# Performance work log

Measured on AMD Instinct MI355X. Metric: run time of the kernel, lower is better.

The kernel has to match this reference:

```python
import jax, jax.numpy as jnp
import numpy as np

HEAD_DIM = 128
HIDDEN = 5120
NUM_KV_GROUPS = 8
NUM_MODALITIES = 3
NUM_Q_HEADS = 40
QKV_PER_MOD = NUM_Q_HEADS * HEAD_DIM + 2 * NUM_KV_GROUPS * HEAD_DIM + NUM_Q_HEADS  # 7208


def _rms_norm(x, w, eps=1e-6):
    xf = x.astype(jnp.float32)
    inv = jax.lax.rsqrt(jnp.mean(xf * xf, axis=-1, keepdims=True) + eps)
    return (xf * inv).astype(x.dtype) * w


def _apply_rope(x, cos, sin):
    # x: [B,S,H,D], cos/sin: [B,S,rd]
    rd = cos.shape[-1]
    xr, xp = x[..., :rd], x[..., rd:]
    c, s = cos[:, :, None, :], sin[:, :, None, :]
    x1, x2 = xr[..., : rd // 2], xr[..., rd // 2:]
    rot = jnp.concatenate([-x2, x1], axis=-1)
    return jnp.concatenate([xr * c + rot * s, xp], axis=-1)


def setup_inputs() -> dict:
    key = jax.random.key(0)
    ks = jax.random.split(key, 6)
    B, S = 1, 2048
    return {
        "x": jax.random.normal(ks[0], (B, S, HIDDEN), jnp.float32),
        "rope_cos": jax.random.uniform(ks[1], (B, S, HEAD_DIM), jnp.float32),
        "rope_sin": jax.random.uniform(ks[2], (B, S, HEAD_DIM), jnp.float32),
        "modality_ids": jax.random.randint(ks[3], (B, S), 0, NUM_MODALITIES, jnp.int32),
        "pre_norm": jnp.ones((NUM_MODALITIES * HIDDEN,), jnp.float32),
        "qkv_w": jax.random.normal(ks[4], (NUM_MODALITIES * QKV_PER_MOD, HIDDEN), jnp.float32) * 0.02,
        "q_norm": jnp.ones((NUM_MODALITIES * HEAD_DIM,), jnp.float32),
        "k_norm": jnp.ones((NUM_MODALITIES * HEAD_DIM,), jnp.float32),
        "proj_w": jax.random.normal(ks[5], (NUM_MODALITIES * HIDDEN, HIDDEN), jnp.float32) * 0.02,
    }


def reference(x, rope_cos, rope_sin, modality_ids, pre_norm, qkv_w, q_norm, k_norm, proj_w):
    B, S, _ = x.shape
    # per-token modality gather of pre-norm weight
    norm_w = pre_norm.reshape(NUM_MODALITIES, HIDDEN)[modality_ids]  # [B,S,H]
    normed = _rms_norm(x, norm_w)

    # modality-routed QKV: compute all modalities, select with one-hot (dense, jit-friendly)
    oh = jax.nn.one_hot(modality_ids, NUM_MODALITIES, dtype=x.dtype)  # [B,S,M]
    qkv_w3 = qkv_w.reshape(NUM_MODALITIES, QKV_PER_MOD, HIDDEN)
    qkv_all = jnp.einsum("bsh,moh->bsmo", normed, qkv_w3)  # [B,S,M,QKV]
    qkv = jnp.einsum("bsm,bsmo->bso", oh, qkv_all)

    q_dim = NUM_Q_HEADS * HEAD_DIM
    k_dim = NUM_KV_GROUPS * HEAD_DIM
    q = qkv[..., :q_dim].reshape(B, S, NUM_Q_HEADS, HEAD_DIM)
    k = qkv[..., q_dim:q_dim + k_dim].reshape(B, S, NUM_KV_GROUPS, HEAD_DIM)
    v = qkv[..., q_dim + k_dim:q_dim + 2 * k_dim].reshape(B, S, NUM_KV_GROUPS, HEAD_DIM)
    gate = jax.nn.sigmoid(qkv[..., q_dim + 2 * k_dim:q_dim + 2 * k_dim + NUM_Q_HEADS])  # [B,S,NQ]

    qn = q_norm.reshape(NUM_MODALITIES, HEAD_DIM)[modality_ids][:, :, None, :]  # [B,S,1,D]
    kn = k_norm.reshape(NUM_MODALITIES, HEAD_DIM)[modality_ids][:, :, None, :]
    q = _rms_norm(q, qn)
    k = _rms_norm(k, kn)

    q = _apply_rope(q, rope_cos, rope_sin)
    k = _apply_rope(k, rope_cos, rope_sin)

    repeat = NUM_Q_HEADS // NUM_KV_GROUPS
    k = jnp.repeat(k, repeat, axis=2)  # [B,S,NQ,D]
    v = jnp.repeat(v, repeat, axis=2)

    scale = 1.0 / np.sqrt(HEAD_DIM)
    scores = jnp.einsum("bqhd,bkhd->bhqk", q, k) * scale  # [B,NQ,S,S]
    attn = jax.nn.softmax(scores, axis=-1)
    out = jnp.einsum("bhqk,bkhd->bqhd", attn, v)  # [B,S,NQ,D]

    out = (out * gate[..., None]).reshape(B, S, NUM_Q_HEADS * HEAD_DIM)

    proj_w3 = proj_w.reshape(NUM_MODALITIES, HIDDEN, HIDDEN)
    proj_all = jnp.einsum("bsh,moh->bsmo", out, proj_w3)  # [B,S,M,H]
    return jnp.einsum("bsm,bsmo->bso", oh, proj_all)
```

## Files before the change

kernel.cpp:

```cpp
#include <hip/hip_runtime.h>

typedef _Float16 f16;
typedef f16 f16x8 __attribute__((ext_vector_type(8)));
typedef f16 f16x4 __attribute__((ext_vector_type(4)));
typedef float f32x4 __attribute__((ext_vector_type(4)));

#define HID 5120
#define QKVO 7208
#define S_TOK 2048
#define NQH 40
#define NKV 8
#define HD 128

__device__ __forceinline__ void gload16(const void* g, void* l) {
    __builtin_amdgcn_global_load_lds(
        (const __attribute__((address_space(1))) void*)g,
        (__attribute__((address_space(3))) void*)l,
        16, 0, 0);
}

__global__ void sort_tokens(const int* __restrict__ mod, int* __restrict__ sorted,
                            int* __restrict__ offs)
{
    int tid = threadIdx.x, wave = tid >> 6, lane = tid & 63;
    int mloc[8];
    int c[3] = {0, 0, 0};
#pragma unroll
    for (int j = 0; j < 8; ++j) {
        int m = mod[tid * 8 + j];
        mloc[j] = m;
        c[m]++;
    }
    __shared__ int wsum[4][3];
    int excl[3];
#pragma unroll
    for (int m = 0; m < 3; ++m) {
        int v = c[m];
        int incl = v;
        for (int d = 1; d < 64; d <<= 1) {
            int n = __shfl_up(incl, d, 64);
            if (lane >= d) incl += n;
        }
        excl[m] = incl - v;
        if (lane == 63) wsum[wave][m] = incl;
    }
    __syncthreads();
    int wbase[3], tot[3];
#pragma unroll
    for (int m = 0; m < 3; ++m) {
        int b = 0, t = 0;
        for (int w = 0; w < 4; ++w) {
            if (w < wave) b += wsum[w][m];
            t += wsum[w][m];
        }
        wbase[m] = b;
        tot[m] = t;
    }
    int base[3];
    base[0] = 0;
    base[1] = tot[0];
    base[2] = tot[0] + tot[1];
    if (tid == 0) {
        offs[0] = 0;
        offs[1] = tot[0];
        offs[2] = tot[0] + tot[1];
        offs[3] = S_TOK;
    }
    int pos[3];
#pragma unroll
    for (int m = 0; m < 3; ++m) pos[m] = base[m] + wbase[m] + excl[m];
#pragma unroll
    for (int j = 0; j < 8; ++j) {
        int m = mloc[j];
        sorted[pos[m]++] = tid * 8 + j;
    }
}

__global__ void cvt_f32_f16(const float* __restrict__ src, f16* __restrict__ dst, int n4)
{
    int i = blockIdx.x * 256 + threadIdx.x;
    int stride = gridDim.x * 256;
    const float4* s4 = (const float4*)src;
    f16x4* d4 = (f16x4*)dst;
    for (; i < n4; i += stride) {
        float4 a = s4[i];
        f16x4 h;
        h[0] = (f16)a.x; h[1] = (f16)a.y; h[2] = (f16)a.z; h[3] = (f16)a.w;
        d4[i] = h;
    }
}

__global__ void rms_pre(const float* __restrict__ x, const int* __restrict__ mod,
                        const float* __restrict__ prenorm, f16* __restrict__ A1)
{
    int tok = blockIdx.x, tid = threadIdx.x;
    int m = mod[tok];
    const float4* xv = (const float4*)(x + (size_t)tok * HID);
    float4 v[5];
    float ss = 0.f;
#pragma unroll
    for (int j = 0; j < 5; ++j) {
        v[j] = xv[tid + 256 * j];
        ss += v[j].x * v[j].x + v[j].y * v[j].y + v[j].z * v[j].z + v[j].w * v[j].w;
    }
    for (int d = 1; d < 64; d <<= 1) ss += __shfl_xor(ss, d, 64);
    __shared__ float ws[4];
    if ((tid & 63) == 0) ws[tid >> 6] = ss;
    __syncthreads();
    float tot = ws[0] + ws[1] + ws[2] + ws[3];
    float inv = rsqrtf(tot * (1.f / HID) + 1e-6f);
    const float4* wv = (const float4*)(prenorm + (size_t)m * HID);
    f16x4* out4 = (f16x4*)(A1 + (size_t)tok * HID);
#pragma unroll
    for (int j = 0; j < 5; ++j) {
        float4 w = wv[tid + 256 * j];
        f16x4 h;
        h[0] = (f16)(v[j].x * inv * w.x);
        h[1] = (f16)(v[j].y * inv * w.y);
        h[2] = (f16)(v[j].z * inv * w.z);
        h[3] = (f16)(v[j].w * inv * w.w);
        out4[tid + 256 * j] = h;
    }
}

__global__ void gemm_grouped(const f16* __restrict__ A, const f16* __restrict__ W,
                             float* __restrict__ C,
                             const int* __restrict__ sorted_tok,
                             const int* __restrict__ mod_off, int NW, int NTN, int NPAN)
{
    const int K = HID;
    int F = blockIdx.x;
    int g = F & 7, s = F >> 3;
    int P = (s >> 4) * 8 + g;
    if (P >= NPAN) return;
    int mt = s & 15;
    int nt = P % NTN, mod = P / NTN;
    int off = mod_off[mod], cnt = mod_off[mod + 1] - off;
    if (mt * 128 >= cnt) return;
    __shared__ __align__(16) f16 As[128 * 64];
    __shared__ __align__(16) f16 Bs[128 * 64];
    __shared__ int rowtok[128];
    int tid = threadIdx.x, wave = tid >> 6, lane = tid & 63;
    if (tid < 128) {
        int r = mt * 128 + tid;
        rowtok[tid] = (r < cnt) ? sorted_tok[off + r] : -1;
    }
    __syncthreads();
    int wr = wave >> 1, wc = wave & 1;
    f32x4 acc[4][4] = {};
    const f16* Wm = W + (size_t)mod * NW * K;
    for (int kt = 0; kt < K / 64; ++kt) {
        int k0 = kt * 64;
#pragma unroll
        for (int it = 0; it < 4; ++it) {
            int c = it * 256 + tid;
            int row = c >> 3, kc = c & 7, skc = kc ^ (row & 7);
            int tk = rowtok[row];
            if (tk < 0) tk = 0;
            gload16(A + (size_t)tk * K + k0 + skc * 8, &As[c * 8]);
        }
#pragma unroll
        for (int it = 0; it < 4; ++it) {
            int c = it * 256 + tid;
            int row = c >> 3, kc = c & 7, skc = kc ^ (row & 7);
            int o = nt * 128 + row;
            if (o >= NW) o = NW - 1;
            gload16(Wm + (size_t)o * K + k0 + skc * 8, &Bs[c * 8]);
        }
        __syncthreads();
#pragma unroll
        for (int ks = 0; ks < 2; ++ks) {
            f16x8 a[4], b[4];
#pragma unroll
            for (int i = 0; i < 4; ++i) {
                int ar = wr * 64 + i * 16 + (lane & 15);
                int ac = (ks * 4 + (lane >> 4)) ^ (ar & 7);
                a[i] = *(const f16x8*)&As[ar * 64 + ac * 8];
                int br = wc * 64 + i * 16 + (lane & 15);
                int bc = (ks * 4 + (lane >> 4)) ^ (br & 7);
                b[i] = *(const f16x8*)&Bs[br * 64 + bc * 8];
            }
#pragma unroll
            for (int mi = 0; mi < 4; ++mi)
#pragma unroll
                for (int nj = 0; nj < 4; ++nj)
                    acc[mi][nj] = __builtin_amdgcn_mfma_f32_16x16x32_f16(
                        a[mi], b[nj], acc[mi][nj], 0, 0, 0);
        }
        __syncthreads();
    }
    int cl = lane & 15, rg = lane >> 4;
#pragma unroll
    for (int mi = 0; mi < 4; ++mi) {
#pragma unroll
        for (int rr = 0; rr < 4; ++rr) {
            int row = wr * 64 + mi * 16 + rg * 4 + rr;
            int tk = rowtok[row];
            if (tk < 0) continue;
            float* crow = C + (size_t)tk * NW;
#pragma unroll
            for (int nj = 0; nj < 4; ++nj) {
                int o = nt * 128 + wc * 64 + nj * 16 + cl;
                if (o < NW) crow[o] = acc[mi][nj][rr];
            }
        }
    }
}

__global__ void qkv_post(const float* __restrict__ qkv, const int* __restrict__ mod,
                         const float* __restrict__ cosb, const float* __restrict__ sinb,
                         const float* __restrict__ qnorm, const float* __restrict__ knorm,
                         f16* __restrict__ Qb, f16* __restrict__ Kb, float* __restrict__ gateb)
{
    int tok = blockIdx.x, tid = threadIdx.x;
    int wave = tid >> 6, lane = tid & 63;
    int m = mod[tok];
    float c0 = cosb[tok * HD + lane], c1 = cosb[tok * HD + 64 + lane];
    float s0 = sinb[tok * HD + lane], s1 = sinb[tok * HD + 64 + lane];
    const float* row = qkv + (size_t)tok * QKVO;
    for (int u = wave; u < 48; u += 4) {
        int base = (u < 40) ? u * HD : NQH * HD + (u - 40) * HD;
        float x0 = row[base + lane];
        float x1 = row[base + 64 + lane];
        float ss = x0 * x0 + x1 * x1;
        for (int d = 1; d < 64; d <<= 1) ss += __shfl_xor(ss, d, 64);
        float inv = rsqrtf(ss * (1.f / HD) + 1e-6f);
        const float* nw = (u < 40 ? qnorm : knorm) + m * HD;
        float n0 = x0 * inv * nw[lane];
        float n1 = x1 * inv * nw[64 + lane];
        float r0 = n0 * c0 - n1 * s0;
        float r1 = n1 * c1 + n0 * s1;
        if (u < 40) {
            const float sc = 0.08838834764831845f;
            r0 *= sc; r1 *= sc;
            Qb[((size_t)u * S_TOK + tok) * HD + lane] = (f16)r0;
            Qb[((size_t)u * S_TOK + tok) * HD + 64 + lane] = (f16)r1;
        } else {
            Kb[((size_t)(u - 40) * S_TOK + tok) * HD + lane] = (f16)r0;
            Kb[((size_t)(u - 40) * S_TOK + tok) * HD + 64 + lane] = (f16)r1;
        }
    }
    if (tid < 40) {
        float g = row[NQH * HD + 2 * NKV * HD + tid];
        gateb[tok * 40 + tid] = 1.f / (1.f + __expf(-g));
    }
}

__global__ void vtrans(const float* __restrict__ qkv, f16* __restrict__ Vt)
{
    int tc = blockIdx.x;
    int g = blockIdx.y;
    int tid = threadIdx.x;
    __shared__ float tile[64][129];
#pragma unroll
    for (int it = 0; it < 8; ++it) {
        int idx = it * 256 + tid;
        int r = idx >> 5, c4 = idx & 31;
        float4 v = *(const float4*)(qkv + (size_t)(tc * 64 + r) * QKVO + NQH * HD + NKV * HD + g * HD + c4 * 4);
        tile[r][c4 * 4 + 0] = v.x;
        tile[r][c4 * 4 + 1] = v.y;
        tile[r][c4 * 4 + 2] = v.z;
        tile[r][c4 * 4 + 3] = v.w;
    }
    __syncthreads();
    int d = tid >> 1, half = tid & 1;
    f16* dst = Vt + ((size_t)g * HD + d) * S_TOK + tc * 64 + half * 32;
#pragma unroll
    for (int j = 0; j < 32; ++j) dst[j] = (f16)tile[half * 32 + j][d];
}

__global__ void attn(const f16* __restrict__ Qb, const f16* __restrict__ Kb,
                     const f16* __restrict__ Vtb, const float* __restrict__ gateb,
                     f16* __restrict__ A2)
{
    int qt = blockIdx.x, h = blockIdx.y, grp = h / 5;
    int tid = threadIdx.x, wave = tid >> 6, lane = tid & 63;
    __shared__ __align__(16) char smem[73728];
    f16* Qs  = (f16*)smem;
    f16* Kb0 = (f16*)(smem + 16384);
    f16* Kb1 = (f16*)smem;
    f16* Vb0 = (f16*)(smem + 32768);
    f16* Vb1 = (f16*)(smem + 49152);
    char* pbase = smem + 65536 + wave * 2048;

    const f16* Qg = Qb + ((size_t)h * S_TOK + qt * 64) * HD;
    const f16* Kg = Kb + (size_t)grp * S_TOK * HD;
    const f16* Vg = Vtb + (size_t)grp * HD * S_TOK;

#pragma unroll
    for (int it = 0; it < 4; ++it) {
        int c = it * 256 + tid, row = c >> 4, kc = c & 15, skc = kc ^ (row & 15);
        gload16(Qg + row * HD + skc * 8, &Qs[c * 8]);
    }
#pragma unroll
    for (int it = 0; it < 4; ++it) {
        int c = it * 256 + tid, row = c >> 4, kc = c & 15, skc = kc ^ (row & 15);
        gload16(Kg + (size_t)row * HD + skc * 8, &Kb0[c * 8]);
    }
#pragma unroll
    for (int it = 0; it < 4; ++it) {
        int c = it * 256 + tid, row = c >> 3, kc = c & 7, skc = kc ^ (row & 7);
        gload16(Vg + (size_t)row * S_TOK + skc * 8, &Vb0[c * 8]);
    }
    asm volatile("s_waitcnt vmcnt(8)" ::: "memory");
    __builtin_amdgcn_s_barrier();
    f16x8 qf[4];
    {
        int row = wave * 16 + (lane & 15);
#pragma unroll
        for (int ks = 0; ks < 4; ++ks) {
            int sk = (ks * 4 + (lane >> 4)) ^ (row & 15);
            qf[ks] = *(const f16x8*)&Qs[row * 128 + sk * 8];
        }
    }
    asm volatile("s_waitcnt lgkmcnt(0)" ::: "memory");
    __builtin_amdgcn_s_barrier();

    f32x4 o[8] = {};
    float mrow[4] = {-3.0e38f, -3.0e38f, -3.0e38f, -3.0e38f};
    float lrow[4] = {0.f, 0.f, 0.f, 0.f};

    int cur = 0;
    for (int t = 0; t < 32; ++t) {
        f16* Ks = cur ? Kb1 : Kb0;
        f16* Vs = cur ? Vb1 : Vb0;
        if (t < 31) {
            f16* Kn = cur ? Kb0 : Kb1;
            f16* Vn = cur ? Vb0 : Vb1;
#pragma unroll
            for (int it = 0; it < 4; ++it) {
                int c = it * 256 + tid, row = c >> 4, kc = c & 15, skc = kc ^ (row & 15);
                gload16(Kg + (size_t)((t + 1) * 64 + row) * HD + skc * 8, &Kn[c * 8]);
            }
#pragma unroll
            for (int it = 0; it < 4; ++it) {
                int c = it * 256 + tid, row = c >> 3, kc = c & 7, skc = kc ^ (row & 7);
                gload16(Vg + (size_t)row * S_TOK + (t + 1) * 64 + skc * 8, &Vn[c * 8]);
            }
            asm volatile("s_waitcnt vmcnt(8)" ::: "memory");
        } else {
            asm volatile("s_waitcnt vmcnt(0)" ::: "memory");
        }
        __builtin_amdgcn_s_barrier();

        f32x4 s[4] = {};
#pragma unroll
        for (int ks = 0; ks < 4; ++ks) {
#pragma unroll
            for (int nj = 0; nj < 4; ++nj) {
                int kr = nj * 16 + (lane & 15);
                int sk = (ks * 4 + (lane >> 4)) ^ (kr & 15);
                f16x8 kf = *(const f16x8*)&Ks[kr * 128 + sk * 8];
                s[nj] = __builtin_amdgcn_mfma_f32_16x16x32_f16(qf[ks], kf, s[nj], 0, 0, 0);
            }
        }
        float mx[4], corr[4], psum[4];
#pragma unroll
        for (int r = 0; r < 4; ++r)
            mx[r] = fmaxf(fmaxf(s[0][r], s[1][r]), fmaxf(s[2][r], s[3][r]));
        for (int d = 1; d < 16; d <<= 1) {
#pragma unroll
            for (int r = 0; r < 4; ++r) mx[r] = fmaxf(mx[r], __shfl_xor(mx[r], d, 16));
        }
#pragma unroll
        for (int r = 0; r < 4; ++r) {
            float mn = fmaxf(mrow[r], mx[r]);
            corr[r] = __expf(mrow[r] - mn);
            mrow[r] = mn;
            psum[r] = 0.f;
        }
#pragma unroll
        for (int nj = 0; nj < 4; ++nj) {
#pragma unroll
            for (int r = 0; r < 4; ++r) {
                float p = __expf(s[nj][r] - mrow[r]);
                psum[r] += p;
                int prow = (lane >> 4) * 4 + r, col = (lane & 15) + nj * 16;
                int addr = (prow * 128 + col * 2) ^ ((prow & 7) << 4);
                *(f16*)(pbase + addr) = (f16)p;
            }
        }
        for (int d = 1; d < 16; d <<= 1) {
#pragma unroll
            for (int r = 0; r < 4; ++r) psum[r] += __shfl_xor(psum[r], d, 16);
        }
#pragma unroll
        for (int r = 0; r < 4; ++r) lrow[r] = lrow[r] * corr[r] + psum[r];
#pragma unroll
        for (int nj2 = 0; nj2 < 8; ++nj2)
#pragma unroll
            for (int r = 0; r < 4; ++r) o[nj2][r] *= corr[r];
#pragma unroll
        for (int ks2 = 0; ks2 < 2; ++ks2) {
            int prow = lane & 15;
            int sk = (ks2 * 4 + (lane >> 4)) ^ (prow & 7);
            f16x8 pa = *(const f16x8*)(pbase + prow * 128 + sk * 16);
#pragma unroll
            for (int nj2 = 0; nj2 < 8; ++nj2) {
                int vr = nj2 * 16 + (lane & 15);
                int skv = (ks2 * 4 + (lane >> 4)) ^ (vr & 7);
                f16x8 vf = *(const f16x8*)&Vs[vr * 64 + skv * 8];
                o[nj2] = __builtin_amdgcn_mfma_f32_16x16x32_f16(pa, vf, o[nj2], 0, 0, 0);
            }
        }
        asm volatile("s_waitcnt lgkmcnt(0)" ::: "memory");
        __builtin_amdgcn_s_barrier();
        cur ^= 1;
    }
    int rbase = qt * 64 + wave * 16 + (lane >> 4) * 4;
#pragma unroll
    for (int r = 0; r < 4; ++r) {
        int tok = rbase + r;
        float sc = gateb[tok * 40 + h] / lrow[r];
#pragma unroll
        for (int nj2 = 0; nj2 < 8; ++nj2) {
            int d = nj2 * 16 + (lane & 15);
            A2[(size_t)tok * HID + h * HD + d] = (f16)(o[nj2][r] * sc);
        }
    }
}

extern "C" void kernel_launch(void* const* d_in, const int* in_sizes, int n_in,
                              void* d_out, int out_size, void* d_ws, size_t ws_size,
                              hipStream_t stream)
{
    const float* x = (const float*)d_in[0];
    const float* rc = (const float*)d_in[1];
    const float* rs = (const float*)d_in[2];
    const int* mod = (const int*)d_in[3];
    const float* prenorm = (const float*)d_in[4];
    const float* qkvw = (const float*)d_in[5];
    const float* qn = (const float*)d_in[6];
    const float* kn = (const float*)d_in[7];
    const float* projw = (const float*)d_in[8];
    float* out = (float*)d_out;

    char* p = (char*)d_ws;
    auto alloc = [&](size_t bytes) {
        char* r = p;
        p += (bytes + 255) & ~(size_t)255;
        return r;
    };
    int* sorted = (int*)alloc(S_TOK * 4);
    int* offs = (int*)alloc(16);
    f16* A1 = (f16*)alloc((size_t)S_TOK * HID * 2);
    f16* Wq = (f16*)alloc((size_t)3 * QKVO * HID * 2);
    f16* Wp = (f16*)alloc((size_t)3 * HID * HID * 2);
    float* qkv = (float*)alloc((size_t)S_TOK * QKVO * 4);
    f16* Qb = (f16*)alloc((size_t)NQH * S_TOK * HD * 2);
    f16* Kb = (f16*)alloc((size_t)NKV * S_TOK * HD * 2);
    f16* Vt = (f16*)alloc((size_t)NKV * HD * S_TOK * 2);
    float* gate = (float*)alloc((size_t)S_TOK * 40 * 4);
    f16* A2 = (f16*)alloc((size_t)S_TOK * HID * 2);
    if ((size_t)(p - (char*)d_ws) > ws_size) return;

    sort_tokens<<<1, 256, 0, stream>>>(mod, sorted, offs);
    cvt_f32_f16<<<2048, 256, 0, stream>>>(qkvw, Wq, 3 * QKVO * HID / 4);
    cvt_f32_f16<<<2048, 256, 0, stream>>>(projw, Wp, 3 * HID * HID / 4);
    rms_pre<<<2048, 256, 0, stream>>>(x, mod, prenorm, A1);
    {
        int NTN = 57, NPAN = NTN * 3;
        int grid = 8 * ((NPAN + 7) / 8) * 16;
        gemm_grouped<<<grid, 256, 0, stream>>>(A1, Wq, qkv, sorted, offs, QKVO, NTN, NPAN);
    }
    qkv_post<<<2048, 256, 0, stream>>>(qkv, mod, rc, rs, qn, kn, Qb, Kb, gate);
    vtrans<<<dim3(32, 8), 256, 0, stream>>>(qkv, Vt);
    attn<<<dim3(32, 40), 256, 0, stream>>>(Qb, Kb, Vt, gate, A2);
    {
        int NTN = 40, NPAN = NTN * 3;
        int grid = 8 * ((NPAN + 7) / 8) * 16;
        gemm_grouped<<<grid, 256, 0, stream>>>(A2, Wp, out, sorted, offs, HID, NTN, NPAN);
    }
}
```

Before: 914.0 us.

## Enlarge grouped GEMM tiles to 256x256, lazily rescale softmax, vectorize P stores

The grouped GEMM moves from 128x128 tiles with 256 threads to 256x256 tiles with 512 threads, and each wave now holds an 8x4 MFMA accumulator block. This raises arithmetic intensity per loaded tile and cuts redundant global loads. The attention kernel skips the running-max rescale unless the new max exceeds the old one by more than 8, and writes P as f16x4 vectors with a permuted column layout. The vtrans output order is changed to match that layout. The risks are register pressure from the 128-float accumulators, lower occupancy, more wasted work on partial tiles, and fp16 overflow headroom in P from the lazy rescale.

```diff
diff --git a/kernel.cpp b/kernel.cpp
--- a/kernel.cpp
+++ b/kernel.cpp
@@ -123,37 +123,38 @@
     }
 }
 
-__global__ void gemm_grouped(const f16* __restrict__ A, const f16* __restrict__ W,
-                             float* __restrict__ C,
-                             const int* __restrict__ sorted_tok,
-                             const int* __restrict__ mod_off, int NW, int NTN, int NPAN)
+__global__ __launch_bounds__(512, 2) void gemm_grouped(
+    const f16* __restrict__ A, const f16* __restrict__ W,
+    float* __restrict__ C,
+    const int* __restrict__ sorted_tok,
+    const int* __restrict__ mod_off, int NW, int NTN, int NPAN)
 {
     const int K = HID;
     int F = blockIdx.x;
     int g = F & 7, s = F >> 3;
-    int P = (s >> 4) * 8 + g;
+    int P = (s >> 3) * 8 + g;
     if (P >= NPAN) return;
-    int mt = s & 15;
+    int mt = s & 7;
     int nt = P % NTN, mod = P / NTN;
     int off = mod_off[mod], cnt = mod_off[mod + 1] - off;
-    if (mt * 128 >= cnt) return;
-    __shared__ __align__(16) f16 As[128 * 64];
-    __shared__ __align__(16) f16 Bs[128 * 64];
-    __shared__ int rowtok[128];
+    if (mt * 256 >= cnt) return;
+    __shared__ __align__(16) f16 As[256 * 64];
+    __shared__ __align__(16) f16 Bs[256 * 64];
+    __shared__ int rowtok[256];
     int tid = threadIdx.x, wave = tid >> 6, lane = tid & 63;
-    if (tid < 128) {
-        int r = mt * 128 + tid;
+    if (tid < 256) {
+        int r = mt * 256 + tid;
         rowtok[tid] = (r < cnt) ? sorted_tok[off + r] : -1;
     }
     __syncthreads();
-    int wr = wave >> 1, wc = wave & 1;
-    f32x4 acc[4][4] = {};
+    int wr = wave >> 2, wc = wave & 3;
+    f32x4 acc[8][4] = {};
     const f16* Wm = W + (size_t)mod * NW * K;
     for (int kt = 0; kt < K / 64; ++kt) {
         int k0 = kt * 64;
 #pragma unroll
         for (int it = 0; it < 4; ++it) {
-            int c = it * 256 + tid;
+            int c = it * 512 + tid;
             int row = c >> 3, kc = c & 7, skc = kc ^ (row & 7);
             int tk = rowtok[row];
             if (tk < 0) tk = 0;
@@ -161,27 +162,30 @@
         }
 #pragma unroll
         for (int it = 0; it < 4; ++it) {
-            int c = it * 256 + tid;
+            int c = it * 512 + tid;
             int row = c >> 3, kc = c & 7, skc = kc ^ (row & 7);
-            int o = nt * 128 + row;
+            int o = nt * 256 + row;
             if (o >= NW) o = NW - 1;
             gload16(Wm + (size_t)o * K + k0 + skc * 8, &Bs[c * 8]);
         }
         __syncthreads();
 #pragma unroll
         for (int ks = 0; ks < 2; ++ks) {
-            f16x8 a[4], b[4];
-#pragma unroll
-            for (int i = 0; i < 4; ++i) {
-                int ar = wr * 64 + i * 16 + (lane & 15);
+            f16x8 a[8], b[4];
+#pragma unroll
+            for (int i = 0; i < 8; ++i) {
+                int ar = wr * 128 + i * 16 + (lane & 15);
                 int ac = (ks * 4 + (lane >> 4)) ^ (ar & 7);
                 a[i] = *(const f16x8*)&As[ar * 64 + ac * 8];
-                int br = wc * 64 + i * 16 + (lane & 15);
+            }
+#pragma unroll
+            for (int j = 0; j < 4; ++j) {
+                int br = wc * 64 + j * 16 + (lane & 15);
                 int bc = (ks * 4 + (lane >> 4)) ^ (br & 7);
-                b[i] = *(const f16x8*)&Bs[br * 64 + bc * 8];
-            }
-#pragma unroll
-            for (int mi = 0; mi < 4; ++mi)
+                b[j] = *(const f16x8*)&Bs[br * 64 + bc * 8];
+            }
+#pragma unroll
+            for (int mi = 0; mi < 8; ++mi)
 #pragma unroll
                 for (int nj = 0; nj < 4; ++nj)
                     acc[mi][nj] = __builtin_amdgcn_mfma_f32_16x16x32_f16(
@@ -191,16 +195,16 @@
     }
     int cl = lane & 15, rg = lane >> 4;
 #pragma unroll
-    for (int mi = 0; mi < 4; ++mi) {
+    for (int mi = 0; mi < 8; ++mi) {
 #pragma unroll
         for (int rr = 0; rr < 4; ++rr) {
-            int row = wr * 64 + mi * 16 + rg * 4 + rr;
+            int row = wr * 128 + mi * 16 + rg * 4 + rr;
             int tk = rowtok[row];
             if (tk < 0) continue;
             float* crow = C + (size_t)tk * NW;
 #pragma unroll
             for (int nj = 0; nj < 4; ++nj) {
-                int o = nt * 128 + wc * 64 + nj * 16 + cl;
+                int o = nt * 256 + wc * 64 + nj * 16 + cl;
                 if (o < NW) crow[o] = acc[mi][nj][rr];
             }
         }
@@ -264,9 +268,12 @@
     }
     __syncthreads();
     int d = tid >> 1, half = tid & 1;
-    f16* dst = Vt + ((size_t)g * HD + d) * S_TOK + tc * 64 + half * 32;
-#pragma unroll
-    for (int j = 0; j < 32; ++j) dst[j] = (f16)tile[half * 32 + j][d];
+    f16* dst = Vt + ((size_t)g * HD + d) * S_TOK + tc * 64;
+#pragma unroll
+    for (int j = 0; j < 32; ++j) {
+        int c = half * 32 + j;
+        dst[c] = (f16)tile[16 * (c & 3) + (c >> 2)][d];
+    }
 }
 
 __global__ void attn(const f16* __restrict__ Qb, const f16* __restrict__ Kb,
@@ -354,7 +361,7 @@
                 s[nj] = __builtin_amdgcn_mfma_f32_16x16x32_f16(qf[ks], kf, s[nj], 0, 0, 0);
             }
         }
-        float mx[4], corr[4], psum[4];
+        float mx[4], psum[4];
 #pragma unroll
         for (int r = 0; r < 4; ++r)
             mx[r] = fmaxf(fmaxf(s[0][r], s[1][r]), fmaxf(s[2][r], s[3][r]));
@@ -362,34 +369,41 @@
 #pragma unroll
             for (int r = 0; r < 4; ++r) mx[r] = fmaxf(mx[r], __shfl_xor(mx[r], d, 16));
         }
+        bool need = false;
+#pragma unroll
+        for (int r = 0; r < 4; ++r) need = need || (mx[r] > mrow[r] + 8.f);
+        if (__any(need)) {
+#pragma unroll
+            for (int r = 0; r < 4; ++r) {
+                float nm = fmaxf(mrow[r], mx[r]);
+                float corr = __expf(mrow[r] - nm);
+                mrow[r] = nm;
+                lrow[r] *= corr;
+#pragma unroll
+                for (int nj2 = 0; nj2 < 8; ++nj2) o[nj2][r] *= corr;
+            }
+        }
+#pragma unroll
+        for (int r = 0; r < 4; ++r) psum[r] = 0.f;
 #pragma unroll
         for (int r = 0; r < 4; ++r) {
-            float mn = fmaxf(mrow[r], mx[r]);
-            corr[r] = __expf(mrow[r] - mn);
-            mrow[r] = mn;
-            psum[r] = 0.f;
-        }
-#pragma unroll
-        for (int nj = 0; nj < 4; ++nj) {
-#pragma unroll
-            for (int r = 0; r < 4; ++r) {
+            f16x4 hp;
+#pragma unroll
+            for (int nj = 0; nj < 4; ++nj) {
                 float p = __expf(s[nj][r] - mrow[r]);
                 psum[r] += p;
-                int prow = (lane >> 4) * 4 + r, col = (lane & 15) + nj * 16;
-                int addr = (prow * 128 + col * 2) ^ ((prow & 7) << 4);
-                *(f16*)(pbase + addr) = (f16)p;
-            }
+                hp[nj] = (f16)p;
+            }
+            int q = (lane >> 4) * 4 + r;
+            int addr = q * 128 + ((8 * (lane & 15)) ^ ((q & 7) << 4));
+            *(f16x4*)(pbase + addr) = hp;
         }
         for (int d = 1; d < 16; d <<= 1) {
 #pragma unroll
             for (int r = 0; r < 4; ++r) psum[r] += __shfl_xor(psum[r], d, 16);
         }
 #pragma unroll
-        for (int r = 0; r < 4; ++r) lrow[r] = lrow[r] * corr[r] + psum[r];
-#pragma unroll
-        for (int nj2 = 0; nj2 < 8; ++nj2)
-#pragma unroll
-            for (int r = 0; r < 4; ++r) o[nj2][r] *= corr[r];
+        for (int r = 0; r < 4; ++r) lrow[r] += psum[r];
 #pragma unroll
         for (int ks2 = 0; ks2 < 2; ++ks2) {
             int prow = lane & 15;
@@ -459,16 +473,16 @@
     cvt_f32_f16<<<2048, 256, 0, stream>>>(projw, Wp, 3 * HID * HID / 4);
     rms_pre<<<2048, 256, 0, stream>>>(x, mod, prenorm, A1);
     {
-        int NTN = 57, NPAN = NTN * 3;
-        int grid = 8 * ((NPAN + 7) / 8) * 16;
-        gemm_grouped<<<grid, 256, 0, stream>>>(A1, Wq, qkv, sorted, offs, QKVO, NTN, NPAN);
+        int NTN = (QKVO + 255) / 256, NPAN = NTN * 3;
+        int grid = ((NPAN + 7) / 8) * 8 * 8;
+        gemm_grouped<<<grid, 512, 0, stream>>>(A1, Wq, qkv, sorted, offs, QKVO, NTN, NPAN);
     }
     qkv_post<<<2048, 256, 0, stream>>>(qkv, mod, rc, rs, qn, kn, Qb, Kb, gate);
     vtrans<<<dim3(32, 8), 256, 0, stream>>>(qkv, Vt);
     attn<<<dim3(32, 40), 256, 0, stream>>>(Qb, Kb, Vt, gate, A2);
     {
-        int NTN = 40, NPAN = NTN * 3;
-        int grid = 8 * ((NPAN + 7) / 8) * 16;
-        gemm_grouped<<<grid, 256, 0, stream>>>(A2, Wp, out, sorted, offs, HID, NTN, NPAN);
-    }
-}
+        int NTN = HID / 256, NPAN = NTN * 3;
+        int grid = ((NPAN + 7) / 8) * 8 * 8;
+        gemm_grouped<<<grid, 512, 0, stream>>>(A2, Wp, out, sorted, offs, HID, NTN, NPAN);
+    }
+}
```

Result: slower. 1.079 ms (+18.1%).

## Load fp32 weights directly in GEMM, lazy softmax rescale, vectorize P stores

Applied to the files above, without the earlier changes.

Drops the separate fp32-to-fp16 weight conversion kernels; the grouped GEMM now streams fp32 weights into shared memory and converts to fp16 when loading fragments, removing a full read/write pass over both weight tensors. Attention only rescales the running max and accumulators when the row max grows by more than a threshold, and writes P as packed f16x4 with a changed column layout. vtrans writes V columns in a permuted token order to match the new P layout. The costs are doubled shared memory and global traffic per B tile in the GEMM, repeated weight conversion by every M-tile that reuses a panel, and a layout coupling between vtrans and the attention P writes.

```diff
diff --git a/kernel.cpp b/kernel.cpp
--- a/kernel.cpp
+++ b/kernel.cpp
@@ -76,20 +76,6 @@
     }
 }
 
-__global__ void cvt_f32_f16(const float* __restrict__ src, f16* __restrict__ dst, int n4)
-{
-    int i = blockIdx.x * 256 + threadIdx.x;
-    int stride = gridDim.x * 256;
-    const float4* s4 = (const float4*)src;
-    f16x4* d4 = (f16x4*)dst;
-    for (; i < n4; i += stride) {
-        float4 a = s4[i];
-        f16x4 h;
-        h[0] = (f16)a.x; h[1] = (f16)a.y; h[2] = (f16)a.z; h[3] = (f16)a.w;
-        d4[i] = h;
-    }
-}
-
 __global__ void rms_pre(const float* __restrict__ x, const int* __restrict__ mod,
                         const float* __restrict__ prenorm, f16* __restrict__ A1)
 {
@@ -123,7 +109,7 @@
     }
 }
 
-__global__ void gemm_grouped(const f16* __restrict__ A, const f16* __restrict__ W,
+__global__ void gemm_grouped(const f16* __restrict__ A, const float* __restrict__ W,
                              float* __restrict__ C,
                              const int* __restrict__ sorted_tok,
                              const int* __restrict__ mod_off, int NW, int NTN, int NPAN)
@@ -138,7 +124,7 @@
     int off = mod_off[mod], cnt = mod_off[mod + 1] - off;
     if (mt * 128 >= cnt) return;
     __shared__ __align__(16) f16 As[128 * 64];
-    __shared__ __align__(16) f16 Bs[128 * 64];
+    __shared__ __align__(16) float Bsf[128 * 64];
     __shared__ int rowtok[128];
     int tid = threadIdx.x, wave = tid >> 6, lane = tid & 63;
     if (tid < 128) {
@@ -148,7 +134,7 @@
     __syncthreads();
     int wr = wave >> 1, wc = wave & 1;
     f32x4 acc[4][4] = {};
-    const f16* Wm = W + (size_t)mod * NW * K;
+    const float* Wm = W + (size_t)mod * NW * K;
     for (int kt = 0; kt < K / 64; ++kt) {
         int k0 = kt * 64;
 #pragma unroll
@@ -160,12 +146,12 @@
             gload16(A + (size_t)tk * K + k0 + skc * 8, &As[c * 8]);
         }
 #pragma unroll
-        for (int it = 0; it < 4; ++it) {
+        for (int it = 0; it < 8; ++it) {
             int c = it * 256 + tid;
-            int row = c >> 3, kc = c & 7, skc = kc ^ (row & 7);
+            int row = c >> 4, kc = c & 15, skc = kc ^ (row & 15);
             int o = nt * 128 + row;
             if (o >= NW) o = NW - 1;
-            gload16(Wm + (size_t)o * K + k0 + skc * 8, &Bs[c * 8]);
+            gload16(Wm + (size_t)o * K + k0 + skc * 4, &Bsf[c * 4]);
         }
         __syncthreads();
 #pragma unroll
@@ -176,9 +162,19 @@
                 int ar = wr * 64 + i * 16 + (lane & 15);
                 int ac = (ks * 4 + (lane >> 4)) ^ (ar & 7);
                 a[i] = *(const f16x8*)&As[ar * 64 + ac * 8];
-                int br = wc * 64 + i * 16 + (lane & 15);
-                int bc = (ks * 4 + (lane >> 4)) ^ (br & 7);
-                b[i] = *(const f16x8*)&Bs[br * 64 + bc * 8];
+            }
+#pragma unroll
+            for (int j = 0; j < 4; ++j) {
+                int br = wc * 64 + j * 16 + (lane & 15);
+                int ch = ks * 4 + (lane >> 4);
+                int s0 = (2 * ch) ^ (br & 15);
+                int s1 = (2 * ch + 1) ^ (br & 15);
+                float4 lo = *(const float4*)&Bsf[br * 64 + s0 * 4];
+                float4 hi = *(const float4*)&Bsf[br * 64 + s1 * 4];
+                f16x8 h;
+                h[0] = (f16)lo.x; h[1] = (f16)lo.y; h[2] = (f16)lo.z; h[3] = (f16)lo.w;
+                h[4] = (f16)hi.x; h[5] = (f16)hi.y; h[6] = (f16)hi.z; h[7] = (f16)hi.w;
+                b[j] = h;
             }
 #pragma unroll
             for (int mi = 0; mi < 4; ++mi)
@@ -264,9 +260,12 @@
     }
     __syncthreads();
     int d = tid >> 1, half = tid & 1;
-    f16* dst = Vt + ((size_t)g * HD + d) * S_TOK + tc * 64 + half * 32;
-#pragma unroll
-    for (int j = 0; j < 32; ++j) dst[j] = (f16)tile[half * 32 + j][d];
+    f16* dst = Vt + ((size_t)g * HD + d) * S_TOK + tc * 64;
+#pragma unroll
+    for (int j = 0; j < 32; ++j) {
+        int c = half * 32 + j;
+        dst[c] = (f16)tile[16 * (c & 3) + (c >> 2)][d];
+    }
 }
 
 __global__ void attn(const f16* __restrict__ Qb, const f16* __restrict__ Kb,
@@ -354,7 +353,7 @@
                 s[nj] = __builtin_amdgcn_mfma_f32_16x16x32_f16(qf[ks], kf, s[nj], 0, 0, 0);
             }
         }
-        float mx[4], corr[4], psum[4];
+        float mx[4], psum[4];
 #pragma unroll
         for (int r = 0; r < 4; ++r)
             mx[r] = fmaxf(fmaxf(s[0][r], s[1][r]), fmaxf(s[2][r], s[3][r]));
@@ -362,34 +361,41 @@
 #pragma unroll
             for (int r = 0; r < 4; ++r) mx[r] = fmaxf(mx[r], __shfl_xor(mx[r], d, 16));
         }
+        bool need = false;
+#pragma unroll
+        for (int r = 0; r < 4; ++r) need = need || (mx[r] > mrow[r] + 8.f);
+        if (__any(need)) {
+#pragma unroll
+            for (int r = 0; r < 4; ++r) {
+                float nm = fmaxf(mrow[r], mx[r]);
+                float corr = __expf(mrow[r] - nm);
+                mrow[r] = nm;
+                lrow[r] *= corr;
+#pragma unroll
+                for (int nj2 = 0; nj2 < 8; ++nj2) o[nj2][r] *= corr;
+            }
+        }
+#pragma unroll
+        for (int r = 0; r < 4; ++r) psum[r] = 0.f;
 #pragma unroll
         for (int r = 0; r < 4; ++r) {
-            float mn = fmaxf(mrow[r], mx[r]);
-            corr[r] = __expf(mrow[r] - mn);
-            mrow[r] = mn;
-            psum[r] = 0.f;
-        }
-#pragma unroll
-        for (int nj = 0; nj < 4; ++nj) {
-#pragma unroll
-            for (int r = 0; r < 4; ++r) {
+            f16x4 hp;
+#pragma unroll
+            for (int nj = 0; nj < 4; ++nj) {
                 float p = __expf(s[nj][r] - mrow[r]);
                 psum[r] += p;
-                int prow = (lane >> 4) * 4 + r, col = (lane & 15) + nj * 16;
-                int addr = (prow * 128 + col * 2) ^ ((prow & 7) << 4);
-                *(f16*)(pbase + addr) = (f16)p;
-            }
+                hp[nj] = (f16)p;
+            }
+            int q = (lane >> 4) * 4 + r;
+            int addr = q * 128 + ((8 * (lane & 15)) ^ ((q & 7) << 4));
+            *(f16x4*)(pbase + addr) = hp;
         }
         for (int d = 1; d < 16; d <<= 1) {
 #pragma unroll
             for (int r = 0; r < 4; ++r) psum[r] += __shfl_xor(psum[r], d, 16);
         }
 #pragma unroll
-        for (int r = 0; r < 4; ++r) lrow[r] = lrow[r] * corr[r] + psum[r];
-#pragma unroll
-        for (int nj2 = 0; nj2 < 8; ++nj2)
-#pragma unroll
-            for (int r = 0; r < 4; ++r) o[nj2][r] *= corr[r];
+        for (int r = 0; r < 4; ++r) lrow[r] += psum[r];
 #pragma unroll
         for (int ks2 = 0; ks2 < 2; ++ks2) {
             int prow = lane & 15;
@@ -444,8 +450,6 @@
     int* sorted = (int*)alloc(S_TOK * 4);
     int* offs = (int*)alloc(16);
     f16* A1 = (f16*)alloc((size_t)S_TOK * HID * 2);
-    f16* Wq = (f16*)alloc((size_t)3 * QKVO * HID * 2);
-    f16* Wp = (f16*)alloc((size_t)3 * HID * HID * 2);
     float* qkv = (float*)alloc((size_t)S_TOK * QKVO * 4);
     f16* Qb = (f16*)alloc((size_t)NQH * S_TOK * HD * 2);
     f16* Kb = (f16*)alloc((size_t)NKV * S_TOK * HD * 2);
@@ -455,13 +459,11 @@
     if ((size_t)(p - (char*)d_ws) > ws_size) return;
 
     sort_tokens<<<1, 256, 0, stream>>>(mod, sorted, offs);
-    cvt_f32_f16<<<2048, 256, 0, stream>>>(qkvw, Wq, 3 * QKVO * HID / 4);
-    cvt_f32_f16<<<2048, 256, 0, stream>>>(projw, Wp, 3 * HID * HID / 4);
     rms_pre<<<2048, 256, 0, stream>>>(x, mod, prenorm, A1);
     {
         int NTN = 57, NPAN = NTN * 3;
         int grid = 8 * ((NPAN + 7) / 8) * 16;
-        gemm_grouped<<<grid, 256, 0, stream>>>(A1, Wq, qkv, sorted, offs, QKVO, NTN, NPAN);
+        gemm_grouped<<<grid, 256, 0, stream>>>(A1, qkvw, qkv, sorted, offs, QKVO, NTN, NPAN);
     }
     qkv_post<<<2048, 256, 0, stream>>>(qkv, mod, rc, rs, qn, kn, Qb, Kb, gate);
     vtrans<<<dim3(32, 8), 256, 0, stream>>>(qkv, Vt);
@@ -469,6 +471,6 @@
     {
         int NTN = 40, NPAN = NTN * 3;
         int grid = 8 * ((NPAN + 7) / 8) * 16;
-        gemm_grouped<<<grid, 256, 0, stream>>>(A2, Wp, out, sorted, offs, HID, NTN, NPAN);
-    }
-}
+        gemm_grouped<<<grid, 256, 0, stream>>>(A2, projw, out, sorted, offs, HID, NTN, NPAN);
+    }
+}
```

Measured after the change: 1.000 ms. +9.4%, slower.
